# Kernel optimization log

Measured on AMD Instinct MI355X. Metric: run time of the kernel, lower is better.

The kernel has to match this reference:

```python
import jax, jax.numpy as jnp
import numpy as np

IN_DIM = 3
OUT_DIM = 3
HIDDEN = [40, 40, 40, 40, 40, 40]
N_POINTS = 2_097_152


def _glorot(key, fan_in, fan_out):
    std = jnp.sqrt(2.0 / (fan_in + fan_out)).astype(jnp.float32)
    return jax.random.normal(key, (fan_in, fan_out), dtype=jnp.float32) * std


def setup_inputs() -> dict:
    key = jax.random.key(0)
    keys = jax.random.split(key, 8)
    coords = jax.random.uniform(keys[0], (N_POINTS, IN_DIM), dtype=jnp.float32)
    dims = [IN_DIM] + HIDDEN + [OUT_DIM]  # [3,40,40,40,40,40,40,3]
    inp = {"coords": coords}
    for i in range(7):
        inp[f"W{i}"] = _glorot(keys[i + 1], dims[i], dims[i + 1])
        inp[f"b{i}"] = jnp.zeros((dims[i + 1],), dtype=jnp.float32)
    return inp


def reference(coords, W0, b0, W1, b1, W2, b2, W3, b3, W4, b4, W5, b5, W6, b6):
    # 7-layer coordinate MLP: Linear+Tanh x6, final Linear. coords: [N,3] -> [N,3]
    Ws = [W0, W1, W2, W3, W4, W5, W6]
    bs = [b0, b1, b2, b3, b4, b5, b6]
    x = coords
    for i in range(6):
        x = jnp.tanh(x @ Ws[i] + bs[i])
    return x @ Ws[6] + bs[6]
```

## Files before the change

kernel.cpp:

```cpp
#include <hip/hip_runtime.h>


typedef _Float16 f16x8 __attribute__((ext_vector_type(8)));
typedef float    f32x16 __attribute__((ext_vector_type(16)));
typedef unsigned int u32x4 __attribute__((ext_vector_type(4)));

#define NFRAG  35
#define TABN   385
#define TABREP 16
#define TABH   0.025f
#define INVH   40.0f
#define TABR   4.8f
#define UOFF   192.0f
#define UMAX   383.999f

__constant__ int INV[48] = {
     0,  1,  2,  3,   8,  9, 10, 11,   4,  5,  6,  7,  12, 13, 14, 15,
    16, 17, 18, 19,  24, 25, 26, 27,  20, 21, 22, 23,  28, 29, 30, 31,
    32, 33, 34, 35,  -1, -1, -1, -1,  36, 37, 38, 39,  -2, -3, -1, -1 };

__global__ void prep_frags(const float* __restrict__ W0, const float* __restrict__ b0,
                           const float* __restrict__ W1, const float* __restrict__ b1,
                           const float* __restrict__ W2, const float* __restrict__ b2,
                           const float* __restrict__ W3, const float* __restrict__ b3,
                           const float* __restrict__ W4, const float* __restrict__ b4,
                           const float* __restrict__ W5, const float* __restrict__ b5,
                           const float* __restrict__ W6, const float* __restrict__ b6,
                           unsigned short* __restrict__ frags,
                           unsigned* __restrict__ table)
{
    int tid = blockIdx.x * 256 + threadIdx.x;

    if (tid < NFRAG * 64) {
        int frag = tid >> 6, lane = tid & 63;

        int layer, mt, ch;
        if (frag < 2)       { layer = 0; mt = frag; ch = 0; }
        else if (frag < 32) { int t = frag - 2; layer = 1 + t / 6; int r = t % 6; mt = r / 3; ch = r % 3; }
        else                { layer = 6; mt = 0; ch = frag - 32; }

        const float* Ws[7] = { W0, W1, W2, W3, W4, W5, W6 };
        const float* bs[7] = { b0, b1, b2, b3, b4, b5, b6 };
        const float* W = Ws[layer];
        const float* b = bs[layer];
        const int fout = (layer == 6) ? 3 : 40;
        const float scale = (layer == 6) ? 1.0f : INVH;

        int jout  = mt * 32 + (lane & 31);
        int kbase = ch * 16 + (lane >> 5) * 8;

        unsigned short h[8];
        for (int i = 0; i < 8; ++i) {
            int k = kbase + i;
            float v = 0.0f;
            if (jout < fout) {
                int jin;
                if (layer == 0) jin = (k < 3) ? k : ((k == 3) ? -2 : ((k == 4) ? -3 : -1));
                else            jin = INV[k];
                if (jin >= 0)       v = W[jin * fout + jout] * scale;
                else if (jin == -2) v = b[jout] * scale;
                else if (jin == -3) v = (layer == 6) ? 0.0f : UOFF;
            }
            _Float16 hv = (_Float16)v;
            h[i] = __builtin_bit_cast(unsigned short, hv);
        }
        unsigned short* dst = frags + frag * 512 + lane * 8;
        for (int i = 0; i < 8; ++i) dst[i] = h[i];
    }
    else if (tid < NFRAG * 64 + TABN) {
        int i = tid - NFRAG * 64;
        float x  = -TABR + (float)i * TABH;
        float t0 = tanhf(x);
        float t1 = tanhf(x + TABH);
        unsigned short bb = __builtin_bit_cast(unsigned short, (_Float16)t0);
        unsigned short dd = __builtin_bit_cast(unsigned short, (_Float16)(t1 - t0));
        unsigned e = (unsigned)bb | ((unsigned)dd << 16);
        for (int r = 0; r < TABREP; ++r) table[i * TABREP + r] = e;
    }
}

__device__ __forceinline__ unsigned int pkf16(float a, float b) {
    return __builtin_bit_cast(unsigned int, __builtin_amdgcn_cvt_pkrtz(a, b));
}
__device__ __forceinline__ f32x16 zf() {
    f32x16 v;
    #pragma unroll
    for (int i = 0; i < 16; ++i) v[i] = 0.0f;
    return v;
}

#define MFMA __builtin_amdgcn_mfma_f32_32x32x16_f16

#define ACT(Da, Db) do {                              \
    Bf[0]  = tl2(Da[0],  Da[1]);                      \
    Bf[1]  = tl2(Da[2],  Da[3]);                      \
    Bf[2]  = tl2(Da[4],  Da[5]);                      \
    Bf[3]  = tl2(Da[6],  Da[7]);                      \
    Bf[4]  = tl2(Da[8],  Da[9]);                      \
    Bf[5]  = tl2(Da[10], Da[11]);                     \
    Bf[6]  = tl2(Da[12], Da[13]);                     \
    Bf[7]  = tl2(Da[14], Da[15]);                     \
    Bf[8]  = tl2(Db[0],  Db[1]);                      \
    Bf[9]  = tl2(Db[2],  Db[3]);                      \
    Bf[10] = PK11;                                    \
    Bf[11] = 0u;                                      \
} while (0)

__global__ __launch_bounds__(512, 4) void mlp_mfma(const float* __restrict__ coords,
                                                   const unsigned short* __restrict__ frags,
                                                   const unsigned* __restrict__ gtab,
                                                   float* __restrict__ out, int npts)
{
    __shared__ __align__(16) unsigned short sf[NFRAG * 512];
    __shared__ __align__(16) unsigned stab[TABN * TABREP];
    {
        const u32x4* s1 = (const u32x4*)frags; u32x4* d1 = (u32x4*)sf;
        for (int i = threadIdx.x; i < NFRAG * 64; i += 512) d1[i] = s1[i];
        const u32x4* s2 = (const u32x4*)gtab;  u32x4* d2 = (u32x4*)stab;
        for (int i = threadIdx.x; i < TABN * TABREP / 4; i += 512) d2[i] = s2[i];
    }
    __syncthreads();

    const int lane = threadIdx.x & 63;
    const int wid  = threadIdx.x >> 6;
    const int p    = (blockIdx.x * 8 + wid) * 32 + (lane & 31);
    const bool valid = (p < npts);

    float c0 = 0.f, c1 = 0.f, c2 = 0.f;
    if (valid) { c0 = coords[p * 3]; c1 = coords[p * 3 + 1]; c2 = coords[p * 3 + 2]; }

    const unsigned int PK11 = pkf16(1.0f, 1.0f);
    const unsigned* __restrict__ tb = stab + (lane & (TABREP - 1));
    const f32x16 CZ = zf();

    auto tl2 = [&](float ua, float ub) -> unsigned {
        ua = __builtin_amdgcn_fmed3f(ua, 0.0f, UMAX);
        ub = __builtin_amdgcn_fmed3f(ub, 0.0f, UMAX);
        float fa = __builtin_amdgcn_fractf(ua);
        float fb = __builtin_amdgcn_fractf(ub);
        unsigned ea = tb[(unsigned)ua * TABREP];
        unsigned eb = tb[(unsigned)ub * TABREP];
        unsigned r;
        asm("v_fma_mixlo_f16 %0, %1, %2, %2 op_sel:[0,1,0] op_sel_hi:[0,1,1]"
            : "=v"(r) : "v"(fa), "v"(ea));
        asm("v_fma_mixhi_f16 %0, %1, %2, %2 op_sel:[0,1,0] op_sel_hi:[0,1,1]"
            : "+v"(r) : "v"(fb), "v"(eb));
        return r;
    };

    unsigned int Bf[12];
    Bf[0] = pkf16(c0, c1);
    Bf[1] = pkf16(c2, 1.0f);
    Bf[2] = pkf16(1.0f, 0.0f);
    Bf[3] = 0u;

    auto AF = [&](int f) -> f16x8 {
        return ((const f16x8*)sf)[f * 64 + lane];
    };
    auto BF = [&](int c) -> f16x8 {
        u32x4 t = { Bf[4 * c + 0], Bf[4 * c + 1], Bf[4 * c + 2], Bf[4 * c + 3] };
        return __builtin_bit_cast(f16x8, t);
    };

    {
        f16x8 bb = BF(0);
        f32x16 D0 = MFMA(AF(0), bb, CZ, 0, 0, 0);
        f32x16 D1 = MFMA(AF(1), bb, CZ, 0, 0, 0);
        ACT(D0, D1);
    }

    #pragma unroll
    for (int l = 1; l <= 5; ++l) {
        const int fb = 2 + (l - 1) * 6;
        f16x8 bc0 = BF(0), bc1 = BF(1), bc2 = BF(2);
        f32x16 D0 = MFMA(AF(fb + 0), bc0, CZ, 0, 0, 0);
        D0 = MFMA(AF(fb + 1), bc1, D0, 0, 0, 0);
        D0 = MFMA(AF(fb + 2), bc2, D0, 0, 0, 0);
        f32x16 D1 = MFMA(AF(fb + 3), bc0, CZ, 0, 0, 0);
        D1 = MFMA(AF(fb + 4), bc1, D1, 0, 0, 0);
        D1 = MFMA(AF(fb + 5), bc2, D1, 0, 0, 0);
        ACT(D0, D1);
    }

    {
        f32x16 D0 = MFMA(AF(32), BF(0), CZ, 0, 0, 0);
        D0 = MFMA(AF(33), BF(1), D0, 0, 0, 0);
        D0 = MFMA(AF(34), BF(2), D0, 0, 0, 0);
        if (lane < 32 && valid) {
            out[p * 3 + 0] = D0[0];
            out[p * 3 + 1] = D0[1];
            out[p * 3 + 2] = D0[2];
        }
    }
}

extern "C" void kernel_launch(void* const* d_in, const int* in_sizes, int n_in,
                              void* d_out, int out_size, void* d_ws, size_t ws_size,
                              hipStream_t stream)
{
    const float* coords = (const float*)d_in[0];
    const float* W0 = (const float*)d_in[1];  const float* b0 = (const float*)d_in[2];
    const float* W1 = (const float*)d_in[3];  const float* b1 = (const float*)d_in[4];
    const float* W2 = (const float*)d_in[5];  const float* b2 = (const float*)d_in[6];
    const float* W3 = (const float*)d_in[7];  const float* b3 = (const float*)d_in[8];
    const float* W4 = (const float*)d_in[9];  const float* b4 = (const float*)d_in[10];
    const float* W5 = (const float*)d_in[11]; const float* b5 = (const float*)d_in[12];
    const float* W6 = (const float*)d_in[13]; const float* b6 = (const float*)d_in[14];
    float* out = (float*)d_out;

    unsigned short* frags = (unsigned short*)d_ws;
    unsigned* table = (unsigned*)((char*)d_ws + NFRAG * 1024);

    const int npts = in_sizes[0] / 3;

    const int prep_threads = NFRAG * 64 + TABN;
    prep_frags<<<(prep_threads + 255) / 256, 256, 0, stream>>>(
        W0, b0, W1, b1, W2, b2, W3, b3, W4, b4, W5, b5, W6, b6, frags, table);

    const int blocks = (npts + 255) / 256;
    mlp_mfma<<<blocks, 512, 0, stream>>>(coords, frags, table, out, npts);
}
```

Before: 122.2 us.

## Process two point tiles per wave and shrink tanh lookup table

Each wave now handles 64 points as two independent 32-point tiles. The weight fragments for a layer are loaded from LDS once and reused for both tiles, and the two MFMA/activation chains interleave to hide latency. The tanh table is shrunk to a coarser range (±3.5, step 1/32) with 32-way replication to cut LDS bank conflicts, and the clamped endpoints are set to saturate. The grid is halved. The trade-offs are higher register pressure and fewer blocks, plus slightly different tanh accuracy near saturation.

```diff
diff --git a/kernel.cpp b/kernel.cpp
--- a/kernel.cpp
+++ b/kernel.cpp
@@ -6,13 +6,12 @@
 typedef unsigned int u32x4 __attribute__((ext_vector_type(4)));
 
 #define NFRAG  35
-#define TABN   385
-#define TABREP 16
-#define TABH   0.025f
-#define INVH   40.0f
-#define TABR   4.8f
-#define UOFF   192.0f
-#define UMAX   383.999f
+#define TABN   225
+#define TABREP 32
+#define INVH   32.0f
+#define UOFF   112.0f
+#define UMAX   223.999f
+#define TABR   3.5f
 
 __constant__ int INV[48] = {
      0,  1,  2,  3,   8,  9, 10, 11,   4,  5,  6,  7,  12, 13, 14, 15,
@@ -69,13 +68,17 @@
     }
     else if (tid < NFRAG * 64 + TABN) {
         int i = tid - NFRAG * 64;
-        float x  = -TABR + (float)i * TABH;
+        const float H = 1.0f / 32.0f;
+        float x  = -TABR + (float)i * H;
         float t0 = tanhf(x);
-        float t1 = tanhf(x + TABH);
-        unsigned short bb = __builtin_bit_cast(unsigned short, (_Float16)t0);
-        unsigned short dd = __builtin_bit_cast(unsigned short, (_Float16)(t1 - t0));
-        unsigned e = (unsigned)bb | ((unsigned)dd << 16);
-        for (int r = 0; r < TABREP; ++r) table[i * TABREP + r] = e;
+        float t1 = tanhf(x + H);
+        float MID = 0.5f * (1.0f + tanhf(TABR));
+        float base = t0, delta = t1 - t0;
+        if (i == 0)        { base = -MID; delta = t1 - base; }
+        if (i == TABN - 2) { delta = MID - t0; }
+        unsigned short bb = __builtin_bit_cast(unsigned short, (_Float16)base);
+        unsigned short dd = __builtin_bit_cast(unsigned short, (_Float16)delta);
+        table[i] = (unsigned)bb | ((unsigned)dd << 16);
     }
 }
 
@@ -91,19 +94,19 @@
 
 #define MFMA __builtin_amdgcn_mfma_f32_32x32x16_f16
 
-#define ACT(Da, Db) do {                              \
-    Bf[0]  = tl2(Da[0],  Da[1]);                      \
-    Bf[1]  = tl2(Da[2],  Da[3]);                      \
-    Bf[2]  = tl2(Da[4],  Da[5]);                      \
-    Bf[3]  = tl2(Da[6],  Da[7]);                      \
-    Bf[4]  = tl2(Da[8],  Da[9]);                      \
-    Bf[5]  = tl2(Da[10], Da[11]);                     \
-    Bf[6]  = tl2(Da[12], Da[13]);                     \
-    Bf[7]  = tl2(Da[14], Da[15]);                     \
-    Bf[8]  = tl2(Db[0],  Db[1]);                      \
-    Bf[9]  = tl2(Db[2],  Db[3]);                      \
-    Bf[10] = PK11;                                    \
-    Bf[11] = 0u;                                      \
+#define ACT(Da, Db, Bfx) do {                         \
+    Bfx[0]  = tl2(Da[0],  Da[1]);                     \
+    Bfx[1]  = tl2(Da[2],  Da[3]);                     \
+    Bfx[2]  = tl2(Da[4],  Da[5]);                     \
+    Bfx[3]  = tl2(Da[6],  Da[7]);                     \
+    Bfx[4]  = tl2(Da[8],  Da[9]);                     \
+    Bfx[5]  = tl2(Da[10], Da[11]);                    \
+    Bfx[6]  = tl2(Da[12], Da[13]);                    \
+    Bfx[7]  = tl2(Da[14], Da[15]);                    \
+    Bfx[8]  = tl2(Db[0],  Db[1]);                     \
+    Bfx[9]  = tl2(Db[2],  Db[3]);                     \
+    Bfx[10] = PK11;                                   \
+    Bfx[11] = 0u;                                     \
 } while (0)
 
 __global__ __launch_bounds__(512, 4) void mlp_mfma(const float* __restrict__ coords,
@@ -116,21 +119,22 @@
     {
         const u32x4* s1 = (const u32x4*)frags; u32x4* d1 = (u32x4*)sf;
         for (int i = threadIdx.x; i < NFRAG * 64; i += 512) d1[i] = s1[i];
-        const u32x4* s2 = (const u32x4*)gtab;  u32x4* d2 = (u32x4*)stab;
-        for (int i = threadIdx.x; i < TABN * TABREP / 4; i += 512) d2[i] = s2[i];
+        for (int i = threadIdx.x; i < TABN * TABREP; i += 512) stab[i] = gtab[i >> 5];
     }
     __syncthreads();
 
     const int lane = threadIdx.x & 63;
     const int wid  = threadIdx.x >> 6;
-    const int p    = (blockIdx.x * 8 + wid) * 32 + (lane & 31);
-    const bool valid = (p < npts);
-
-    float c0 = 0.f, c1 = 0.f, c2 = 0.f;
-    if (valid) { c0 = coords[p * 3]; c1 = coords[p * 3 + 1]; c2 = coords[p * 3 + 2]; }
+    const int pA   = (blockIdx.x * 8 + wid) * 64 + (lane & 31);
+    const int pB   = pA + 32;
+    const bool vA = (pA < npts), vB = (pB < npts);
+
+    float cA0 = 0.f, cA1 = 0.f, cA2 = 0.f, cB0 = 0.f, cB1 = 0.f, cB2 = 0.f;
+    if (vA) { cA0 = coords[pA * 3]; cA1 = coords[pA * 3 + 1]; cA2 = coords[pA * 3 + 2]; }
+    if (vB) { cB0 = coords[pB * 3]; cB1 = coords[pB * 3 + 1]; cB2 = coords[pB * 3 + 2]; }
 
     const unsigned int PK11 = pkf16(1.0f, 1.0f);
-    const unsigned* __restrict__ tb = stab + (lane & (TABREP - 1));
+    const unsigned* __restrict__ tb = stab + (lane & 31);
     const f32x16 CZ = zf();
 
     auto tl2 = [&](float ua, float ub) -> unsigned {
@@ -148,48 +152,80 @@
         return r;
     };
 
-    unsigned int Bf[12];
-    Bf[0] = pkf16(c0, c1);
-    Bf[1] = pkf16(c2, 1.0f);
-    Bf[2] = pkf16(1.0f, 0.0f);
-    Bf[3] = 0u;
+    unsigned int BfA[12], BfB[12];
+    BfA[0] = pkf16(cA0, cA1); BfA[1] = pkf16(cA2, 1.0f);
+    BfA[2] = pkf16(1.0f, 0.0f); BfA[3] = 0u;
+    BfB[0] = pkf16(cB0, cB1); BfB[1] = pkf16(cB2, 1.0f);
+    BfB[2] = pkf16(1.0f, 0.0f); BfB[3] = 0u;
 
     auto AF = [&](int f) -> f16x8 {
         return ((const f16x8*)sf)[f * 64 + lane];
     };
-    auto BF = [&](int c) -> f16x8 {
-        u32x4 t = { Bf[4 * c + 0], Bf[4 * c + 1], Bf[4 * c + 2], Bf[4 * c + 3] };
+    auto BFx = [&](const unsigned (&B)[12], int c) -> f16x8 {
+        u32x4 t = { B[4 * c + 0], B[4 * c + 1], B[4 * c + 2], B[4 * c + 3] };
         return __builtin_bit_cast(f16x8, t);
     };
 
-    {
-        f16x8 bb = BF(0);
-        f32x16 D0 = MFMA(AF(0), bb, CZ, 0, 0, 0);
-        f32x16 D1 = MFMA(AF(1), bb, CZ, 0, 0, 0);
-        ACT(D0, D1);
+    f16x8 F0, F1, F2, F3, F4, F5;
+
+    F0 = AF(0); F1 = AF(1);
+    {
+        f32x16 D0 = MFMA(F0, BFx(BfA, 0), CZ, 0, 0, 0);
+        f32x16 D1 = MFMA(F1, BFx(BfA, 0), CZ, 0, 0, 0);
+        ACT(D0, D1, BfA);
+    }
+    {
+        f32x16 D0 = MFMA(F0, BFx(BfB, 0), CZ, 0, 0, 0);
+        f32x16 D1 = MFMA(F1, BFx(BfB, 0), CZ, 0, 0, 0);
+        ACT(D0, D1, BfB);
     }
 
     #pragma unroll
     for (int l = 1; l <= 5; ++l) {
         const int fb = 2 + (l - 1) * 6;
-        f16x8 bc0 = BF(0), bc1 = BF(1), bc2 = BF(2);
-        f32x16 D0 = MFMA(AF(fb + 0), bc0, CZ, 0, 0, 0);
-        D0 = MFMA(AF(fb + 1), bc1, D0, 0, 0, 0);
-        D0 = MFMA(AF(fb + 2), bc2, D0, 0, 0, 0);
-        f32x16 D1 = MFMA(AF(fb + 3), bc0, CZ, 0, 0, 0);
-        D1 = MFMA(AF(fb + 4), bc1, D1, 0, 0, 0);
-        D1 = MFMA(AF(fb + 5), bc2, D1, 0, 0, 0);
-        ACT(D0, D1);
-    }
-
-    {
-        f32x16 D0 = MFMA(AF(32), BF(0), CZ, 0, 0, 0);
-        D0 = MFMA(AF(33), BF(1), D0, 0, 0, 0);
-        D0 = MFMA(AF(34), BF(2), D0, 0, 0, 0);
-        if (lane < 32 && valid) {
-            out[p * 3 + 0] = D0[0];
-            out[p * 3 + 1] = D0[1];
-            out[p * 3 + 2] = D0[2];
+        F0 = AF(fb + 0); F1 = AF(fb + 1); F2 = AF(fb + 2);
+        F3 = AF(fb + 3); F4 = AF(fb + 4); F5 = AF(fb + 5);
+        {
+            f16x8 B0 = BFx(BfA, 0), B1 = BFx(BfA, 1), B2 = BFx(BfA, 2);
+            f32x16 D0 = MFMA(F0, B0, CZ, 0, 0, 0);
+            D0 = MFMA(F1, B1, D0, 0, 0, 0);
+            D0 = MFMA(F2, B2, D0, 0, 0, 0);
+            f32x16 D1 = MFMA(F3, B0, CZ, 0, 0, 0);
+            D1 = MFMA(F4, B1, D1, 0, 0, 0);
+            D1 = MFMA(F5, B2, D1, 0, 0, 0);
+            ACT(D0, D1, BfA);
+        }
+        {
+            f16x8 B0 = BFx(BfB, 0), B1 = BFx(BfB, 1), B2 = BFx(BfB, 2);
+            f32x16 D0 = MFMA(F0, B0, CZ, 0, 0, 0);
+            D0 = MFMA(F1, B1, D0, 0, 0, 0);
+            D0 = MFMA(F2, B2, D0, 0, 0, 0);
+            f32x16 D1 = MFMA(F3, B0, CZ, 0, 0, 0);
+            D1 = MFMA(F4, B1, D1, 0, 0, 0);
+            D1 = MFMA(F5, B2, D1, 0, 0, 0);
+            ACT(D0, D1, BfB);
+        }
+    }
+
+    F0 = AF(32); F1 = AF(33); F2 = AF(34);
+    {
+        f32x16 D0 = MFMA(F0, BFx(BfA, 0), CZ, 0, 0, 0);
+        D0 = MFMA(F1, BFx(BfA, 1), D0, 0, 0, 0);
+        D0 = MFMA(F2, BFx(BfA, 2), D0, 0, 0, 0);
+        if (lane < 32 && vA) {
+            out[pA * 3 + 0] = D0[0];
+            out[pA * 3 + 1] = D0[1];
+            out[pA * 3 + 2] = D0[2];
+        }
+    }
+    {
+        f32x16 D0 = MFMA(F0, BFx(BfB, 0), CZ, 0, 0, 0);
+        D0 = MFMA(F1, BFx(BfB, 1), D0, 0, 0, 0);
+        D0 = MFMA(F2, BFx(BfB, 2), D0, 0, 0, 0);
+        if (lane < 32 && vB) {
+            out[pB * 3 + 0] = D0[0];
+            out[pB * 3 + 1] = D0[1];
+            out[pB * 3 + 2] = D0[2];
         }
     }
 }
@@ -217,6 +253,6 @@
     prep_frags<<<(prep_threads + 255) / 256, 256, 0, stream>>>(
         W0, b0, W1, b1, W2, b2, W3, b3, W4, b4, W5, b5, W6, b6, frags, table);
 
-    const int blocks = (npts + 255) / 256;
+    const int blocks = (npts + 511) / 512;
     mlp_mfma<<<blocks, 512, 0, stream>>>(coords, frags, table, out, npts);
 }
```

Measured after the change: 118.8 us. -2.7%, faster.
